# Kernel tuning notes

Hardware: AMD Instinct MI355X
Metric: run time of the kernel (lower is better)

## Reference

```python
import jax, jax.numpy as jnp
import numpy as np
import math

EMBED = 256
NH = 8            # num_heads
HD = EMBED // NH  # head_dim = 32
LEVELS = 4
P = 4             # points per level
SUMP = LEVELS * P # 16
OFFSET_SCALE = 0.5
SPATIAL = ((80, 80), (40, 40), (20, 20), (10, 10))  # (H, W) per level
BS, LQ = 4, 4096
LV = sum(h * w for h, w in SPATIAL)  # 8500


def _offset_bias():
    # replicates _reset_parameters grid init for sampling_offsets.bias
    thetas = np.arange(NH, dtype=np.float32) * (2.0 * math.pi / NH)
    grid = np.stack([np.cos(thetas), np.sin(thetas)], -1)  # [NH,2]
    grid = grid / np.abs(grid).max(-1, keepdims=True)
    grid = np.tile(grid.reshape(NH, 1, 2), (1, SUMP, 1))   # [NH,SUMP,2]
    scaling = np.concatenate([np.arange(1, P + 1) for _ in range(LEVELS)]).reshape(1, SUMP, 1)
    grid = grid * scaling
    return jnp.asarray(grid.reshape(-1), dtype=jnp.float32)  # [NH*SUMP*2]


def setup_inputs() -> dict:
    key = jax.random.key(0)
    ks = jax.random.split(key, 8)
    xavier = lambda k, fi, fo: jax.random.uniform(k, (fi, fo), jnp.float32,
                                                  -math.sqrt(6.0 / (fi + fo)), math.sqrt(6.0 / (fi + fo)))
    return {
        "query": jax.random.normal(ks[0], (BS, LQ, EMBED), jnp.float32),
        "reference_points": jax.random.uniform(ks[1], (BS, LQ, 1, 4), jnp.float32),
        "value": jax.random.normal(ks[2], (BS, LV, EMBED), jnp.float32),
        # sampling_offsets: weight is zero-init in torch; use small random so offsets depend on query
        "W_off": jax.random.normal(ks[3], (EMBED, NH * SUMP * 2), jnp.float32) * 0.01,
        "b_off": _offset_bias(),
        "W_attn": jax.random.normal(ks[4], (EMBED, NH * SUMP), jnp.float32) * 0.01,
        "b_attn": jnp.zeros((NH * SUMP,), jnp.float32),
        "W_v": xavier(ks[5], EMBED, EMBED),
        "b_v": jnp.zeros((EMBED,), jnp.float32),
        "W_o": xavier(ks[6], EMBED, EMBED),
        "b_o": jnp.zeros((EMBED,), jnp.float32),
    }


def _bilinear_sample(v_l, loc, Hl, Wl):
    """grid_sample (bilinear, zero padding, align_corners=False) on one level.
    v_l: [bs, NH, Hl*Wl, HD]; loc: [bs, Lq, NH, P, 2] in [0,1] (x=width, y=height).
    Returns [bs, Lq, NH, P, HD]."""
    bs, lq, nh, p, _ = loc.shape
    x = loc[..., 0] * Wl - 0.5
    y = loc[..., 1] * Hl - 0.5
    x0 = jnp.floor(x)
    y0 = jnp.floor(y)
    lx, ly = x - x0, y - y0
    x0i = x0.astype(jnp.int32)
    y0i = y0.astype(jnp.int32)

    def corner(xi, yi, w):
        valid = ((xi >= 0) & (xi < Wl) & (yi >= 0) & (yi < Hl)).astype(v_l.dtype)
        idx = jnp.clip(yi, 0, Hl - 1) * Wl + jnp.clip(xi, 0, Wl - 1)  # [bs,Lq,NH,P]
        idx = jnp.transpose(idx, (0, 2, 1, 3)).reshape(bs, nh, lq * p)
        g = jnp.take_along_axis(v_l, idx[..., None], axis=2)          # [bs,NH,Lq*P,HD]
        g = g.reshape(bs, nh, lq, p, HD).transpose(0, 2, 1, 3, 4)     # [bs,Lq,NH,P,HD]
        return g * (w * valid)[..., None]

    return (corner(x0i, y0i, (1 - lx) * (1 - ly))
            + corner(x0i + 1, y0i, lx * (1 - ly))
            + corner(x0i, y0i + 1, (1 - lx) * ly)
            + corner(x0i + 1, y0i + 1, lx * ly))


def reference(query, reference_points, value, W_off, b_off, W_attn, b_attn, W_v, b_v, W_o, b_o):
    bs, lq = query.shape[:2]
    lv = value.shape[1]

    v = (value @ W_v + b_v).reshape(bs, lv, NH, HD)

    off = (query @ W_off + b_off).reshape(bs, lq, NH, SUMP, 2)
    attn = jax.nn.softmax((query @ W_attn + b_attn).reshape(bs, lq, NH, SUMP), axis=-1)

    # reference_points last dim == 4 path (box refs)
    nps = jnp.full((SUMP, 1), 1.0 / P, dtype=query.dtype)  # num_points_scale
    loc = (reference_points[:, :, None, :, :2]
           + off * nps * reference_points[:, :, None, :, 2:] * OFFSET_SCALE)  # [bs,Lq,NH,SUMP,2]

    out = jnp.zeros((bs, lq, NH, HD), dtype=query.dtype)
    v_start, p_start = 0, 0
    for (Hl, Wl) in SPATIAL:
        n = Hl * Wl
        v_l = jnp.transpose(v[:, v_start:v_start + n], (0, 2, 1, 3))  # [bs,NH,n,HD]
        loc_l = loc[:, :, :, p_start:p_start + P]
        w_l = attn[:, :, :, p_start:p_start + P]
        sampled = _bilinear_sample(v_l, loc_l, Hl, Wl)                # [bs,Lq,NH,P,HD]
        out = out + jnp.einsum('blhpd,blhp->blhd', sampled, w_l)
        v_start += n
        p_start += P

    return out.reshape(bs, lq, EMBED) @ W_o + b_o
```

## Files before the change

kernel.cpp:

```cpp
#include <hip/hip_runtime.h>

#define NH 8
#define HD 32
#define SUMP 16
#define LQ 4096
#define BS 4
#define LV 8500
#define NQ (BS * LQ)
#define MV (BS * LV)

typedef float f32x4 __attribute__((ext_vector_type(4)));
typedef _Float16 f16x8 __attribute__((ext_vector_type(8)));
typedef _Float16 f16x2 __attribute__((ext_vector_type(2)));

__global__ __launch_bounds__(256) void prep_kernel(
    const float* __restrict__ Wv, const float* __restrict__ Woff,
    const float* __restrict__ Wattn, const float* __restrict__ Wo,
    const float* __restrict__ boff, const float* __restrict__ battn,
    _Float16* __restrict__ WtVf, _Float16* __restrict__ WtOAf,
    _Float16* __restrict__ WtOf, float* __restrict__ biasOA)
{
    int g = blockIdx.x * 256 + threadIdx.x;
    int gl; _Float16* dst; int which;
    if (g < 65536)       { gl = g;          dst = WtVf;  which = 0; }
    else if (g < 163840) { gl = g - 65536;  dst = WtOAf; which = 1; }
    else                 { gl = g - 163840; dst = WtOf;  which = 2; }
    int e = gl & 7, m16 = (gl >> 3) & 15, q = (gl >> 7) & 3, C = (gl >> 9) & 7, T = gl >> 12;
    int n = T * 16 + m16, k = C * 32 + q * 8 + e;
    float w;
    if (which == 0)      w = Wv[k * 256 + n];
    else if (which == 1) w = (n < 256) ? Woff[k * 256 + n] : Wattn[k * 128 + (n - 256)];
    else                 w = Wo[k * 256 + n];
    dst[gl] = (_Float16)w;
    if (blockIdx.x == 0) biasOA[threadIdx.x] = boff[threadIdx.x];
    if (blockIdx.x == 1 && threadIdx.x < 128) biasOA[256 + threadIdx.x] = battn[threadIdx.x];
}

__device__ __forceinline__ f16x8 cvt8(const float4& lo, const float4& hi) {
    f16x8 r;
    r[0] = (_Float16)lo.x; r[1] = (_Float16)lo.y; r[2] = (_Float16)lo.z; r[3] = (_Float16)lo.w;
    r[4] = (_Float16)hi.x; r[5] = (_Float16)hi.y; r[6] = (_Float16)hi.z; r[7] = (_Float16)hi.w;
    return r;
}

template <int NI, bool V_MODE, bool A_F16>
__device__ __forceinline__ void chunk_gemm(
    const float* __restrict__ A32, const _Float16* __restrict__ A16,
    const _Float16* __restrict__ Bf, const float* __restrict__ bias,
    void* __restrict__ Cv, int M, int N, int mchunk, int ntbase,
    _Float16* __restrict__ As )
{
    const int t = threadIdx.x;
    const int wave = t >> 6, lane = t & 63;
    const int quad = lane >> 4, l16 = lane & 15;

    {
        const int srow = t >> 2, schunk = t & 3;
        int gr = mchunk * 64 + srow;
        if (gr > M - 1) gr = M - 1;
        if (A_F16) {
            const _Float16* src = A16 + (size_t)gr * 256 + schunk * 64;
            f16x8 hb[8];
            #pragma unroll
            for (int j = 0; j < 8; ++j) hb[j] = *(const f16x8*)(src + j * 8);
            #pragma unroll
            for (int j = 0; j < 8; ++j) {
                int slot = (schunk * 8 + j) ^ (srow & 7);
                *(f16x8*)(As + srow * 256 + slot * 8) = hb[j];
            }
        } else {
            const float* src = A32 + (size_t)gr * 256 + schunk * 64;
            float4 buf[16];
            #pragma unroll
            for (int j = 0; j < 16; ++j) buf[j] = *(const float4*)(src + j * 4);
            #pragma unroll
            for (int j = 0; j < 8; ++j) {
                f16x8 h = cvt8(buf[2 * j], buf[2 * j + 1]);
                int slot = (schunk * 8 + j) ^ (srow & 7);
                *(f16x8*)(As + srow * 256 + slot * 8) = h;
            }
        }
    }
    __syncthreads();

    const int ntile0 = ntbase + wave * NI;
    const _Float16* bp[NI];
    #pragma unroll
    for (int ni = 0; ni < NI; ++ni)
        bp[ni] = Bf + (size_t)(ntile0 + ni) * 4096 + lane * 8;

    f16x8 bcur[NI], bnxt[NI];
    f32x4 acc[4][NI] = {};
    #pragma unroll
    for (int ni = 0; ni < NI; ++ni) bcur[ni] = *(const f16x8*)(bp[ni]);

    #pragma unroll
    for (int k = 0; k < 8; ++k) {
        if (k < 7) {
            #pragma unroll
            for (int ni = 0; ni < NI; ++ni) bnxt[ni] = *(const f16x8*)(bp[ni] + (k + 1) * 512);
        }
        f16x8 af[4];
        #pragma unroll
        for (int mi = 0; mi < 4; ++mi) {
            int row = mi * 16 + l16;
            int slot = (quad + k * 4) ^ (row & 7);
            af[mi] = *(const f16x8*)(As + row * 256 + slot * 8);
        }
        #pragma unroll
        for (int mi = 0; mi < 4; ++mi)
            #pragma unroll
            for (int ni = 0; ni < NI; ++ni)
                acc[mi][ni] = __builtin_amdgcn_mfma_f32_16x16x32_f16(af[mi], bcur[ni], acc[mi][ni], 0, 0, 0);
        if (k < 7) {
            #pragma unroll
            for (int ni = 0; ni < NI; ++ni) bcur[ni] = bnxt[ni];
        }
    }

    if (V_MODE) {
        #pragma unroll
        for (int mi = 0; mi < 4; ++mi) {
            int mq = mchunk * 64 + mi * 16 + quad * 4;
            size_t rb[4]; int vld[4];
            #pragma unroll
            for (int r = 0; r < 4; ++r) {
                int m = mq + r;
                vld[r] = (m < M);
                int mm = vld[r] ? m : 0;
                int b = mm / LV; int pos = mm - b * LV;
                rb[r] = ((size_t)b * NH * LV + pos) * 32;
            }
            #pragma unroll
            for (int ni = 0; ni < NI; ++ni) {
                int n = (ntile0 + ni) * 16 + l16;
                float bv = bias[n];
                int h = n >> 5, d = n & 31;
                size_t ho = (size_t)h * (LV * 32) + d;
                #pragma unroll
                for (int r = 0; r < 4; ++r)
                    if (vld[r]) ((_Float16*)Cv)[rb[r] + ho] = (_Float16)(acc[mi][ni][r] + bv);
            }
        }
    } else {
        #pragma unroll
        for (int ni = 0; ni < NI; ++ni) {
            int n = (ntile0 + ni) * 16 + l16;
            float bv = bias[n];
            #pragma unroll
            for (int mi = 0; mi < 4; ++mi) {
                int mq = mchunk * 64 + mi * 16 + quad * 4;
                #pragma unroll
                for (int r = 0; r < 4; ++r)
                    ((float*)Cv)[(size_t)(mq + r) * N + n] = acc[mi][ni][r] + bv;
            }
        }
    }
}

__global__ __launch_bounds__(256) void gemm_dual_kernel(
    const float* __restrict__ value, const _Float16* __restrict__ WtVf,
    const float* __restrict__ b_v, _Float16* __restrict__ v_f16,
    const float* __restrict__ query, const _Float16* __restrict__ WtOAf,
    const float* __restrict__ biasOA, float* __restrict__ oa)
{
    __shared__ __align__(16) _Float16 As[64 * 256];
    int bid = blockIdx.x;
    if (bid < 532) {
        chunk_gemm<4, true, false>(value, nullptr, WtVf, b_v, v_f16, MV, 256,
                                   bid, 0, As);
    } else {
        int g = bid - 532;
        chunk_gemm<3, false, false>(query, nullptr, WtOAf, biasOA, oa, NQ, 384,
                                    g >> 1, (g & 1) * 12, As);
    }
}

__global__ __launch_bounds__(256) void gemm_o_kernel(
    const _Float16* __restrict__ mid, const _Float16* __restrict__ WtOf,
    const float* __restrict__ b_o, float* __restrict__ out)
{
    __shared__ __align__(16) _Float16 As[32 * 256];
    const int t = threadIdx.x;
    const int wave = t >> 6, lane = t & 63;
    const int quad = lane >> 4, l16 = lane & 15;
    const int mchunk = blockIdx.x >> 1;
    const int nc = blockIdx.x & 1;

    {
        const int srow = t >> 3, sc = t & 7;
        const _Float16* src = mid + (size_t)(mchunk * 32 + srow) * 256 + sc * 32;
        f16x8 hb[4];
        #pragma unroll
        for (int j = 0; j < 4; ++j) hb[j] = *(const f16x8*)(src + j * 8);
        #pragma unroll
        for (int j = 0; j < 4; ++j) {
            int slot = (sc * 4 + j) ^ (srow & 7);
            *(f16x8*)(As + srow * 256 + slot * 8) = hb[j];
        }
    }
    __syncthreads();

    const int wrow = wave >> 1, wcol = wave & 1;
    const int ntile0 = nc * 8 + wcol * 4;
    const _Float16* bp[4];
    #pragma unroll
    for (int ni = 0; ni < 4; ++ni)
        bp[ni] = WtOf + (size_t)(ntile0 + ni) * 4096 + lane * 8;

    f16x8 bcur[4], bnxt[4];
    f32x4 acc[4] = {};
    #pragma unroll
    for (int ni = 0; ni < 4; ++ni) bcur[ni] = *(const f16x8*)(bp[ni]);

    #pragma unroll
    for (int k = 0; k < 8; ++k) {
        if (k < 7) {
            #pragma unroll
            for (int ni = 0; ni < 4; ++ni) bnxt[ni] = *(const f16x8*)(bp[ni] + (k + 1) * 512);
        }
        const int row = wrow * 16 + l16;
        const int slot = (quad + k * 4) ^ (row & 7);
        f16x8 af = *(const f16x8*)(As + row * 256 + slot * 8);
        #pragma unroll
        for (int ni = 0; ni < 4; ++ni)
            acc[ni] = __builtin_amdgcn_mfma_f32_16x16x32_f16(af, bcur[ni], acc[ni], 0, 0, 0);
        if (k < 7) {
            #pragma unroll
            for (int ni = 0; ni < 4; ++ni) bcur[ni] = bnxt[ni];
        }
    }

    #pragma unroll
    for (int ni = 0; ni < 4; ++ni) {
        int n = (ntile0 + ni) * 16 + l16;
        float bv = b_o[n];
        int mq = mchunk * 32 + wrow * 16 + quad * 4;
        #pragma unroll
        for (int r = 0; r < 4; ++r)
            out[(size_t)(mq + r) * 256 + n] = acc[ni][r] + bv;
    }
}

__global__ void sample_kernel(
    const _Float16* __restrict__ v,
    const float* __restrict__ oa,
    const float* __restrict__ refp,
    _Float16* __restrict__ mid)
{
    const int blk = blockIdx.x;
    const int xcd = blk & 7, j = blk >> 3;
    const int bh = xcd * 4 + (j & 3);
    const int chunk = j >> 2;
    const int b = bh >> 3, h = bh & 7;
    const int rowG0 = b * LQ + chunk * 16;

    const int t = threadIdx.x;
    const int wave = t >> 6, lane = t & 63;

    __shared__ __align__(16) int2   s_pk[16 * 17];
    __shared__ __align__(16) int2   s_w2[16 * 17];
    __shared__ __align__(16) float  s_part[2 * 8 * 32];

    {
        int task = t >> 4, p = t & 15, l = p >> 2;
        int row = rowG0 + task;
        float4 r4 = *(const float4*)(refp + (size_t)row * 4);
        float2 o2 = *(const float2*)(oa + (size_t)row * 384 + (h * 16 + p) * 2);
        float raw = oa[(size_t)row * 384 + 256 + h * 16 + p];

        float mx = raw;
        #pragma unroll
        for (int d = 8; d >= 1; d >>= 1) mx = fmaxf(mx, __shfl_xor(mx, d, 16));
        float ex = __expf(raw - mx);
        float sm = ex;
        #pragma unroll
        for (int d = 8; d >= 1; d >>= 1) sm += __shfl_xor(sm, d, 16);
        float w = ex * __builtin_amdgcn_rcpf(sm);

        int Wl = 80 >> l;
        int vst = (l == 0) ? 0 : (l == 1) ? 6400 : (l == 2) ? 8000 : 8400;
        float x = (r4.x + o2.x * 0.125f * r4.z) * Wl - 0.5f;
        float y = (r4.y + o2.y * 0.125f * r4.w) * Wl - 0.5f;
        float x0f = floorf(x), y0f = floorf(y);
        float lx = x - x0f, ly = y - y0f;
        int x0 = (int)x0f, y0 = (int)y0f;
        int x1 = x0 + 1, y1 = y0 + 1;
        float mx0 = (x0 >= 0 && x0 < Wl) ? 1.f : 0.f;
        float mx1 = (x1 >= 0 && x1 < Wl) ? 1.f : 0.f;
        float my0 = (y0 >= 0 && y0 < Wl) ? 1.f : 0.f;
        float my1 = (y1 >= 0 && y1 < Wl) ? 1.f : 0.f;
        int cx0 = min(max(x0, 0), Wl - 1), cx1 = min(max(x1, 0), Wl - 1);
        int cy0 = min(max(y0, 0), Wl - 1), cy1 = min(max(y1, 0), Wl - 1);
        int2 r_pk;
        r_pk.x = (vst + cy0 * Wl + cx0) * 64;
        r_pk.y = ((cx1 - cx0) * 64) | (((cy1 - cy0) * Wl * 64) << 16);
        f16x2 wxy, wzw;
        wxy[0] = (_Float16)(w * (1.f - lx) * (1.f - ly) * mx0 * my0);
        wxy[1] = (_Float16)(w * lx * (1.f - ly) * mx1 * my0);
        wzw[0] = (_Float16)(w * (1.f - lx) * ly * mx0 * my1);
        wzw[1] = (_Float16)(w * lx * ly * mx1 * my1);
        int2 r_w2;
        r_w2.x = __builtin_bit_cast(int, wxy);
        r_w2.y = __builtin_bit_cast(int, wzw);
        int s = task * 17 + p;
        s_pk[s] = r_pk; s_w2[s] = r_w2;
    }
    __syncthreads();

    {
        const int wg = wave >> 1, wp = wave & 1;
        const int pgl = lane >> 5, tk = (lane >> 2) & 7, dv2 = lane & 3;
        const int task = wg * 8 + tk;
        const int row = rowG0 + task;
        const char* vb = (const char*)v + ((size_t)(b * NH + h) * LV) * 64 + dv2 * 16;

        int2 pk[4]; f16x2 wxy[4], wzw[4];
        #pragma unroll
        for (int jj = 0; jj < 4; ++jj) {
            int p = jj * 4 + wp * 2 + pgl;
            int s = task * 17 + p;
            pk[jj] = s_pk[s];
            int2 w2 = s_w2[s];
            wxy[jj] = __builtin_bit_cast(f16x2, w2.x);
            wzw[jj] = __builtin_bit_cast(f16x2, w2.y);
        }
        f16x8 g0[4], g1[4], g2[4], g3[4];
        #pragma unroll
        for (int jj = 0; jj < 4; ++jj) {
            int dx = pk[jj].y & 0xffff, dy = pk[jj].y >> 16;
            const char* base = vb + pk[jj].x;
            g0[jj] = *(const f16x8*)(base);
            g1[jj] = *(const f16x8*)(base + dx);
            g2[jj] = *(const f16x8*)(base + dy);
            g3[jj] = *(const f16x8*)(base + dx + dy);
        }
        float acc8[8] = {};
        #pragma unroll
        for (int jj = 0; jj < 4; ++jj)
            #pragma unroll
            for (int c = 0; c < 8; ++c) {
                f16x2 ga; ga[0] = g0[jj][c]; ga[1] = g1[jj][c];
                f16x2 gb; gb[0] = g2[jj][c]; gb[1] = g3[jj][c];
                acc8[c] = __builtin_amdgcn_fdot2(ga, wxy[jj], acc8[c], false);
                acc8[c] = __builtin_amdgcn_fdot2(gb, wzw[jj], acc8[c], false);
            }

        #pragma unroll
        for (int c = 0; c < 8; ++c) acc8[c] += __shfl_xor(acc8[c], 32, 64);
        if (wp == 1 && lane < 32) {
            #pragma unroll
            for (int c = 0; c < 8; ++c) s_part[wg * 256 + c * 32 + lane] = acc8[c];
        }
        __syncthreads();
        if (wp == 0 && lane < 32) {
            f16x8 m8;
            #pragma unroll
            for (int c = 0; c < 8; ++c)
                m8[c] = (_Float16)(acc8[c] + s_part[wg * 256 + c * 32 + lane]);
            *(f16x8*)(mid + (size_t)row * 256 + h * 32 + dv2 * 8) = m8;
        }
    }
}

extern "C" void kernel_launch(void* const* d_in, const int* in_sizes, int n_in,
                              void* d_out, int out_size, void* d_ws, size_t ws_size,
                              hipStream_t stream) {
    const float* query  = (const float*)d_in[0];
    const float* refp   = (const float*)d_in[1];
    const float* value  = (const float*)d_in[2];
    const float* W_off  = (const float*)d_in[3];
    const float* b_off  = (const float*)d_in[4];
    const float* W_attn = (const float*)d_in[5];
    const float* b_attn = (const float*)d_in[6];
    const float* W_v    = (const float*)d_in[7];
    const float* b_v    = (const float*)d_in[8];
    const float* W_o    = (const float*)d_in[9];
    const float* b_o    = (const float*)d_in[10];

    char* ws = (char*)d_ws;
    _Float16* v_f16  = (_Float16*)(ws + 0);
    float*    oa_f32 = (float*)(ws + 17408000);
    _Float16* mid    = (_Float16*)(ws + 42573824);
    _Float16* WtVf   = (_Float16*)(ws + 50962432);
    _Float16* WtOAf  = (_Float16*)(ws + 51093504);
    _Float16* WtOf   = (_Float16*)(ws + 51290112);
    float*    biasOA = (float*)(ws + 51421184);

    prep_kernel<<<896, 256, 0, stream>>>(W_v, W_off, W_attn, W_o, b_off, b_attn,
                                         WtVf, WtOAf, WtOf, biasOA);
    gemm_dual_kernel<<<1044, 256, 0, stream>>>(
        value, WtVf, b_v, v_f16, query, WtOAf, biasOA, oa_f32);
    sample_kernel<<<8192, 256, 0, stream>>>(v_f16, oa_f32, refp, mid);
    gemm_o_kernel<<<1024, 256, 0, stream>>>(mid, WtOf, b_o, (float*)d_out);
}
```

Measured before the change: 164.9 us.

## Use 32-row GEMM tiles with full-N per block, unify output GEMM

The shared chunk GEMM now works on 32-row A tiles instead of 64. Each block covers the full N width, looping over multiple passes for the offset/attention GEMM so the A tile is loaded only once. The value projection gets twice as many blocks for better occupancy and less shared memory per block. The output GEMM reuses the same routine with 512 blocks that each cover all 256 columns, instead of splitting N across two blocks that both reload A. In exchange, B-weight reuse per block drops and the query GEMM runs its passes serially.

```diff
diff --git a/kernel.cpp b/kernel.cpp
--- a/kernel.cpp
+++ b/kernel.cpp
@@ -43,11 +43,11 @@
     return r;
 }
 
-template <int NI, bool V_MODE, bool A_F16>
-__device__ __forceinline__ void chunk_gemm(
+template <int NI, int NPASS, bool V_MODE, bool A_F16>
+__device__ __forceinline__ void chunk_gemm32(
     const float* __restrict__ A32, const _Float16* __restrict__ A16,
     const _Float16* __restrict__ Bf, const float* __restrict__ bias,
-    void* __restrict__ Cv, int M, int N, int mchunk, int ntbase,
+    void* __restrict__ Cv, int M, int N, int mchunk,
     _Float16* __restrict__ As )
 {
     const int t = threadIdx.x;
@@ -55,104 +55,107 @@
     const int quad = lane >> 4, l16 = lane & 15;
 
     {
-        const int srow = t >> 2, schunk = t & 3;
-        int gr = mchunk * 64 + srow;
+        const int srow = t >> 3, sc = t & 7;
+        int gr = mchunk * 32 + srow;
         if (gr > M - 1) gr = M - 1;
         if (A_F16) {
-            const _Float16* src = A16 + (size_t)gr * 256 + schunk * 64;
-            f16x8 hb[8];
-            #pragma unroll
-            for (int j = 0; j < 8; ++j) hb[j] = *(const f16x8*)(src + j * 8);
-            #pragma unroll
-            for (int j = 0; j < 8; ++j) {
-                int slot = (schunk * 8 + j) ^ (srow & 7);
+            const _Float16* src = A16 + (size_t)gr * 256 + sc * 32;
+            f16x8 hb[4];
+            #pragma unroll
+            for (int j = 0; j < 4; ++j) hb[j] = *(const f16x8*)(src + j * 8);
+            #pragma unroll
+            for (int j = 0; j < 4; ++j) {
+                int slot = (sc * 4 + j) ^ (srow & 7);
                 *(f16x8*)(As + srow * 256 + slot * 8) = hb[j];
             }
         } else {
-            const float* src = A32 + (size_t)gr * 256 + schunk * 64;
-            float4 buf[16];
-            #pragma unroll
-            for (int j = 0; j < 16; ++j) buf[j] = *(const float4*)(src + j * 4);
-            #pragma unroll
-            for (int j = 0; j < 8; ++j) {
-                f16x8 h = cvt8(buf[2 * j], buf[2 * j + 1]);
-                int slot = (schunk * 8 + j) ^ (srow & 7);
-                *(f16x8*)(As + srow * 256 + slot * 8) = h;
+            const float* src = A32 + (size_t)gr * 256 + sc * 32;
+            float4 buf[8];
+            #pragma unroll
+            for (int j = 0; j < 8; ++j) buf[j] = *(const float4*)(src + j * 4);
+            #pragma unroll
+            for (int j = 0; j < 4; ++j) {
+                f16x8 hcv = cvt8(buf[2 * j], buf[2 * j + 1]);
+                int slot = (sc * 4 + j) ^ (srow & 7);
+                *(f16x8*)(As + srow * 256 + slot * 8) = hcv;
             }
         }
     }
     __syncthreads();
 
-    const int ntile0 = ntbase + wave * NI;
-    const _Float16* bp[NI];
     #pragma unroll
-    for (int ni = 0; ni < NI; ++ni)
-        bp[ni] = Bf + (size_t)(ntile0 + ni) * 4096 + lane * 8;
-
-    f16x8 bcur[NI], bnxt[NI];
-    f32x4 acc[4][NI] = {};
-    #pragma unroll
-    for (int ni = 0; ni < NI; ++ni) bcur[ni] = *(const f16x8*)(bp[ni]);
-
-    #pragma unroll
-    for (int k = 0; k < 8; ++k) {
-        if (k < 7) {
-            #pragma unroll
-            for (int ni = 0; ni < NI; ++ni) bnxt[ni] = *(const f16x8*)(bp[ni] + (k + 1) * 512);
-        }
-        f16x8 af[4];
-        #pragma unroll
-        for (int mi = 0; mi < 4; ++mi) {
-            int row = mi * 16 + l16;
-            int slot = (quad + k * 4) ^ (row & 7);
-            af[mi] = *(const f16x8*)(As + row * 256 + slot * 8);
-        }
-        #pragma unroll
-        for (int mi = 0; mi < 4; ++mi)
-            #pragma unroll
-            for (int ni = 0; ni < NI; ++ni)
-                acc[mi][ni] = __builtin_amdgcn_mfma_f32_16x16x32_f16(af[mi], bcur[ni], acc[mi][ni], 0, 0, 0);
-        if (k < 7) {
-            #pragma unroll
-            for (int ni = 0; ni < NI; ++ni) bcur[ni] = bnxt[ni];
-        }
-    }
-
-    if (V_MODE) {
-        #pragma unroll
-        for (int mi = 0; mi < 4; ++mi) {
-            int mq = mchunk * 64 + mi * 16 + quad * 4;
-            size_t rb[4]; int vld[4];
-            #pragma unroll
-            for (int r = 0; r < 4; ++r) {
-                int m = mq + r;
-                vld[r] = (m < M);
-                int mm = vld[r] ? m : 0;
-                int b = mm / LV; int pos = mm - b * LV;
-                rb[r] = ((size_t)b * NH * LV + pos) * 32;
-            }
+    for (int pass = 0; pass < NPASS; ++pass) {
+        const int ntile0 = pass * (4 * NI) + wave * NI;
+        const _Float16* bp[NI];
+        #pragma unroll
+        for (int ni = 0; ni < NI; ++ni)
+            bp[ni] = Bf + (size_t)(ntile0 + ni) * 4096 + lane * 8;
+
+        f16x8 bcur[NI], bnxt[NI];
+        f32x4 acc[2][NI] = {};
+        #pragma unroll
+        for (int ni = 0; ni < NI; ++ni) bcur[ni] = *(const f16x8*)(bp[ni]);
+
+        #pragma unroll
+        for (int k = 0; k < 8; ++k) {
+            if (k < 7) {
+                #pragma unroll
+                for (int ni = 0; ni < NI; ++ni) bnxt[ni] = *(const f16x8*)(bp[ni] + (k + 1) * 512);
+            }
+            f16x8 af[2];
+            #pragma unroll
+            for (int mi = 0; mi < 2; ++mi) {
+                int row = mi * 16 + l16;
+                int slot = (quad + k * 4) ^ (row & 7);
+                af[mi] = *(const f16x8*)(As + row * 256 + slot * 8);
+            }
+            #pragma unroll
+            for (int mi = 0; mi < 2; ++mi)
+                #pragma unroll
+                for (int ni = 0; ni < NI; ++ni)
+                    acc[mi][ni] = __builtin_amdgcn_mfma_f32_16x16x32_f16(af[mi], bcur[ni], acc[mi][ni], 0, 0, 0);
+            if (k < 7) {
+                #pragma unroll
+                for (int ni = 0; ni < NI; ++ni) bcur[ni] = bnxt[ni];
+            }
+        }
+
+        if (V_MODE) {
+            #pragma unroll
+            for (int mi = 0; mi < 2; ++mi) {
+                int mq = mchunk * 32 + mi * 16 + quad * 4;
+                size_t rb[4]; int vld[4];
+                #pragma unroll
+                for (int r = 0; r < 4; ++r) {
+                    int m = mq + r;
+                    vld[r] = (m < M);
+                    int mm = vld[r] ? m : 0;
+                    int b = mm / LV; int pos = mm - b * LV;
+                    rb[r] = ((size_t)b * NH * LV + pos) * 32;
+                }
+                #pragma unroll
+                for (int ni = 0; ni < NI; ++ni) {
+                    int n = (ntile0 + ni) * 16 + l16;
+                    float bv = bias[n];
+                    int h = n >> 5, d = n & 31;
+                    size_t ho = (size_t)h * (LV * 32) + d;
+                    #pragma unroll
+                    for (int r = 0; r < 4; ++r)
+                        if (vld[r]) ((_Float16*)Cv)[rb[r] + ho] = (_Float16)(acc[mi][ni][r] + bv);
+                }
+            }
+        } else {
             #pragma unroll
             for (int ni = 0; ni < NI; ++ni) {
                 int n = (ntile0 + ni) * 16 + l16;
                 float bv = bias[n];
-                int h = n >> 5, d = n & 31;
-                size_t ho = (size_t)h * (LV * 32) + d;
-                #pragma unroll
-                for (int r = 0; r < 4; ++r)
-                    if (vld[r]) ((_Float16*)Cv)[rb[r] + ho] = (_Float16)(acc[mi][ni][r] + bv);
-            }
-        }
-    } else {
-        #pragma unroll
-        for (int ni = 0; ni < NI; ++ni) {
-            int n = (ntile0 + ni) * 16 + l16;
-            float bv = bias[n];
-            #pragma unroll
-            for (int mi = 0; mi < 4; ++mi) {
-                int mq = mchunk * 64 + mi * 16 + quad * 4;
-                #pragma unroll
-                for (int r = 0; r < 4; ++r)
-                    ((float*)Cv)[(size_t)(mq + r) * N + n] = acc[mi][ni][r] + bv;
+                #pragma unroll
+                for (int mi = 0; mi < 2; ++mi) {
+                    int mq = mchunk * 32 + mi * 16 + quad * 4;
+                    #pragma unroll
+                    for (int r = 0; r < 4; ++r)
+                        ((float*)Cv)[(size_t)(mq + r) * N + n] = acc[mi][ni][r] + bv;
+                }
             }
         }
     }
@@ -164,15 +167,14 @@
     const float* __restrict__ query, const _Float16* __restrict__ WtOAf,
     const float* __restrict__ biasOA, float* __restrict__ oa)
 {
-    __shared__ __align__(16) _Float16 As[64 * 256];
+    __shared__ __align__(16) _Float16 As[32 * 256];
     int bid = blockIdx.x;
-    if (bid < 532) {
-        chunk_gemm<4, true, false>(value, nullptr, WtVf, b_v, v_f16, MV, 256,
-                                   bid, 0, As);
+    if (bid < 1063) {
+        chunk_gemm32<4, 1, true, false>(value, nullptr, WtVf, b_v, v_f16, MV, 256,
+                                        bid, As);
     } else {
-        int g = bid - 532;
-        chunk_gemm<3, false, false>(query, nullptr, WtOAf, biasOA, oa, NQ, 384,
-                                    g >> 1, (g & 1) * 12, As);
+        chunk_gemm32<3, 2, false, false>(query, nullptr, WtOAf, biasOA, oa, NQ, 384,
+                                         bid - 1063, As);
     }
 }
 
@@ -181,65 +183,8 @@
     const float* __restrict__ b_o, float* __restrict__ out)
 {
     __shared__ __align__(16) _Float16 As[32 * 256];
-    const int t = threadIdx.x;
-    const int wave = t >> 6, lane = t & 63;
-    const int quad = lane >> 4, l16 = lane & 15;
-    const int mchunk = blockIdx.x >> 1;
-    const int nc = blockIdx.x & 1;
-
-    {
-        const int srow = t >> 3, sc = t & 7;
-        const _Float16* src = mid + (size_t)(mchunk * 32 + srow) * 256 + sc * 32;
-        f16x8 hb[4];
-        #pragma unroll
-        for (int j = 0; j < 4; ++j) hb[j] = *(const f16x8*)(src + j * 8);
-        #pragma unroll
-        for (int j = 0; j < 4; ++j) {
-            int slot = (sc * 4 + j) ^ (srow & 7);
-            *(f16x8*)(As + srow * 256 + slot * 8) = hb[j];
-        }
-    }
-    __syncthreads();
-
-    const int wrow = wave >> 1, wcol = wave & 1;
-    const int ntile0 = nc * 8 + wcol * 4;
-    const _Float16* bp[4];
-    #pragma unroll
-    for (int ni = 0; ni < 4; ++ni)
-        bp[ni] = WtOf + (size_t)(ntile0 + ni) * 4096 + lane * 8;
-
-    f16x8 bcur[4], bnxt[4];
-    f32x4 acc[4] = {};
-    #pragma unroll
-    for (int ni = 0; ni < 4; ++ni) bcur[ni] = *(const f16x8*)(bp[ni]);
-
-    #pragma unroll
-    for (int k = 0; k < 8; ++k) {
-        if (k < 7) {
-            #pragma unroll
-            for (int ni = 0; ni < 4; ++ni) bnxt[ni] = *(const f16x8*)(bp[ni] + (k + 1) * 512);
-        }
-        const int row = wrow * 16 + l16;
-        const int slot = (quad + k * 4) ^ (row & 7);
-        f16x8 af = *(const f16x8*)(As + row * 256 + slot * 8);
-        #pragma unroll
-        for (int ni = 0; ni < 4; ++ni)
-            acc[ni] = __builtin_amdgcn_mfma_f32_16x16x32_f16(af, bcur[ni], acc[ni], 0, 0, 0);
-        if (k < 7) {
-            #pragma unroll
-            for (int ni = 0; ni < 4; ++ni) bcur[ni] = bnxt[ni];
-        }
-    }
-
-    #pragma unroll
-    for (int ni = 0; ni < 4; ++ni) {
-        int n = (ntile0 + ni) * 16 + l16;
-        float bv = b_o[n];
-        int mq = mchunk * 32 + wrow * 16 + quad * 4;
-        #pragma unroll
-        for (int r = 0; r < 4; ++r)
-            out[(size_t)(mq + r) * 256 + n] = acc[ni][r] + bv;
-    }
+    chunk_gemm32<4, 1, false, true>(nullptr, mid, WtOf, b_o, out, NQ, 256,
+                                    blockIdx.x, As);
 }
 
 __global__ void sample_kernel(
@@ -389,8 +334,8 @@
 
     prep_kernel<<<896, 256, 0, stream>>>(W_v, W_off, W_attn, W_o, b_off, b_attn,
                                          WtVf, WtOAf, WtOf, biasOA);
-    gemm_dual_kernel<<<1044, 256, 0, stream>>>(
+    gemm_dual_kernel<<<1575, 256, 0, stream>>>(
         value, WtVf, b_v, v_f16, query, WtOAf, biasOA, oa_f32);
     sample_kernel<<<8192, 256, 0, stream>>>(v_f16, oa_f32, refp, mid);
-    gemm_o_kernel<<<1024, 256, 0, stream>>>(mid, WtOf, b_o, (float*)d_out);
-}
+    gemm_o_kernel<<<512, 256, 0, stream>>>(mid, WtOf, b_o, (float*)d_out);
+}
```

New measurement: 168.0 us. About the same (+1.9%).

## Store sampled output in MFMA fragment layout and drop LDS staging in output GEMM

Applied to the files above, without the earlier changes.

The sampling kernel now writes its fp16 intermediate in a tiled layout that matches the 16x16x32 MFMA A-operand fragment order. The output projection GEMM can then load A fragments straight from global memory with coalesced 16-byte loads, with no LDS staging and no __syncthreads. Each wave computes its own 32x32 output tile with register double-buffering of both A and B. The trade-off is more redundant global/L2 reads of the A and B fragments across waves, since nothing is shared through LDS any more.

```diff
diff --git a/kernel.cpp b/kernel.cpp
--- a/kernel.cpp
+++ b/kernel.cpp
@@ -177,68 +177,59 @@
 }
 
 __global__ __launch_bounds__(256) void gemm_o_kernel(
-    const _Float16* __restrict__ mid, const _Float16* __restrict__ WtOf,
+    const _Float16* __restrict__ midf, const _Float16* __restrict__ WtOf,
     const float* __restrict__ b_o, float* __restrict__ out)
 {
-    __shared__ __align__(16) _Float16 As[32 * 256];
-    const int t = threadIdx.x;
-    const int wave = t >> 6, lane = t & 63;
+    const int lane = threadIdx.x & 63;
     const int quad = lane >> 4, l16 = lane & 15;
-    const int mchunk = blockIdx.x >> 1;
-    const int nc = blockIdx.x & 1;
-
-    {
-        const int srow = t >> 3, sc = t & 7;
-        const _Float16* src = mid + (size_t)(mchunk * 32 + srow) * 256 + sc * 32;
-        f16x8 hb[4];
-        #pragma unroll
-        for (int j = 0; j < 4; ++j) hb[j] = *(const f16x8*)(src + j * 8);
-        #pragma unroll
-        for (int j = 0; j < 4; ++j) {
-            int slot = (sc * 4 + j) ^ (srow & 7);
-            *(f16x8*)(As + srow * 256 + slot * 8) = hb[j];
-        }
-    }
-    __syncthreads();
-
-    const int wrow = wave >> 1, wcol = wave & 1;
-    const int ntile0 = nc * 8 + wcol * 4;
-    const _Float16* bp[4];
-    #pragma unroll
-    for (int ni = 0; ni < 4; ++ni)
-        bp[ni] = WtOf + (size_t)(ntile0 + ni) * 4096 + lane * 8;
-
-    f16x8 bcur[4], bnxt[4];
-    f32x4 acc[4] = {};
-    #pragma unroll
-    for (int ni = 0; ni < 4; ++ni) bcur[ni] = *(const f16x8*)(bp[ni]);
-
+    const int g = blockIdx.x * 4 + (threadIdx.x >> 6);
+    const int mt = (g >> 3) * 2;
+    const int nt = (g & 7) * 2;
+
+    const _Float16* ap[2];
+    const _Float16* bp[2];
+    #pragma unroll
+    for (int i = 0; i < 2; ++i) {
+        ap[i] = midf + (size_t)(mt + i) * 4096 + lane * 8;
+        bp[i] = WtOf + (size_t)(nt + i) * 4096 + lane * 8;
+    }
+    f16x8 aC[2], bC[2], aN[2], bN[2];
+    f32x4 acc[2][2] = {};
+    #pragma unroll
+    for (int i = 0; i < 2; ++i) {
+        aC[i] = *(const f16x8*)(ap[i]);
+        bC[i] = *(const f16x8*)(bp[i]);
+    }
     #pragma unroll
     for (int k = 0; k < 8; ++k) {
         if (k < 7) {
             #pragma unroll
-            for (int ni = 0; ni < 4; ++ni) bnxt[ni] = *(const f16x8*)(bp[ni] + (k + 1) * 512);
-        }
-        const int row = wrow * 16 + l16;
-        const int slot = (quad + k * 4) ^ (row & 7);
-        f16x8 af = *(const f16x8*)(As + row * 256 + slot * 8);
-        #pragma unroll
-        for (int ni = 0; ni < 4; ++ni)
-            acc[ni] = __builtin_amdgcn_mfma_f32_16x16x32_f16(af, bcur[ni], acc[ni], 0, 0, 0);
+            for (int i = 0; i < 2; ++i) {
+                aN[i] = *(const f16x8*)(ap[i] + (k + 1) * 512);
+                bN[i] = *(const f16x8*)(bp[i] + (k + 1) * 512);
+            }
+        }
+        #pragma unroll
+        for (int mi = 0; mi < 2; ++mi)
+            #pragma unroll
+            for (int ni = 0; ni < 2; ++ni)
+                acc[mi][ni] = __builtin_amdgcn_mfma_f32_16x16x32_f16(aC[mi], bC[ni], acc[mi][ni], 0, 0, 0);
         if (k < 7) {
             #pragma unroll
-            for (int ni = 0; ni < 4; ++ni) bcur[ni] = bnxt[ni];
-        }
-    }
-
-    #pragma unroll
-    for (int ni = 0; ni < 4; ++ni) {
-        int n = (ntile0 + ni) * 16 + l16;
+            for (int i = 0; i < 2; ++i) { aC[i] = aN[i]; bC[i] = bN[i]; }
+        }
+    }
+    #pragma unroll
+    for (int ni = 0; ni < 2; ++ni) {
+        int n = (nt + ni) * 16 + l16;
         float bv = b_o[n];
-        int mq = mchunk * 32 + wrow * 16 + quad * 4;
-        #pragma unroll
-        for (int r = 0; r < 4; ++r)
-            out[(size_t)(mq + r) * 256 + n] = acc[ni][r] + bv;
+        #pragma unroll
+        for (int mi = 0; mi < 2; ++mi) {
+            int mq = (mt + mi) * 16 + quad * 4;
+            #pragma unroll
+            for (int r = 0; r < 4; ++r)
+                out[(size_t)(mq + r) * 256 + n] = acc[mi][ni][r] + bv;
+        }
     }
 }
 
@@ -246,7 +237,7 @@
     const _Float16* __restrict__ v,
     const float* __restrict__ oa,
     const float* __restrict__ refp,
-    _Float16* __restrict__ mid)
+    _Float16* __restrict__ midf)
 {
     const int blk = blockIdx.x;
     const int xcd = blk & 7, j = blk >> 3;
@@ -358,7 +349,8 @@
             #pragma unroll
             for (int c = 0; c < 8; ++c)
                 m8[c] = (_Float16)(acc8[c] + s_part[wg * 256 + c * 32 + lane]);
-            *(f16x8*)(mid + (size_t)row * 256 + h * 32 + dv2 * 8) = m8;
+            *(f16x8*)(midf + ((size_t)(row >> 4) * 8 + h) * 512
+                           + ((row & 15) + 16 * dv2) * 8) = m8;
         }
     }
 }
```

Result: no change. 164.9 us (-0.0%).
